# Performance work log

Hardware: AMD Instinct MI355X
Metric: run time of the kernel (lower is better)

The kernel has to match this reference:

```python
import jax, jax.numpy as jnp
import numpy as np

E, N, D, DFF, NE = 8, 4096, 1024, 2048, 65536

def setup_inputs() -> dict:
    key = jax.random.key(0)
    k1, k2, k3, k4 = jax.random.split(key, 4)
    x = jax.random.normal(k1, (E, N, D), dtype=jnp.float32)
    W1 = jax.random.normal(k2, (E, D, DFF), dtype=jnp.float32) * (1.0 / np.sqrt(D))
    W2 = jax.random.normal(k3, (E, DFF, D), dtype=jnp.float32) * (1.0 / np.sqrt(DFF))
    edge_index = jax.random.randint(k4, (2, NE), 0, N, dtype=jnp.int64)
    return {"x": x, "W1": W1, "W2": W2, "edge_index": edge_index}

def reference(x, W1, W2, edge_index):
    # Vectorized form of the per-expert Python loop + stack:
    # each expert: h = relu(x_e @ W1_e); agg[dst] += h[src]; out_e = agg @ W2_e
    n = x.shape[1]
    src, dst = edge_index[0], edge_index[1]
    h = jax.nn.relu(jnp.einsum('end,edf->enf', x, W1))  # [e, n, dff]
    msgs = h[:, src, :]                                  # [e, n_edges, dff] (irregular gather)
    agg = jax.vmap(lambda m: jax.ops.segment_sum(m, dst, num_segments=n))(msgs)  # [e, n, dff]
    out = jnp.einsum('enf,efd->end', agg, W2)            # [e, n, d] == x.shape
    return out
```

## Files before the change

kernel.cpp:

```cpp
#include <hip/hip_runtime.h>

#define E_ 8
#define N_ 4096
#define D_ 1024
#define DFF_ 2048
#define NE_ 65536

typedef __attribute__((ext_vector_type(8))) short short8;
typedef __attribute__((ext_vector_type(4))) float f32x4;

__device__ __forceinline__ unsigned short f2bf(float f) {
  unsigned u = __float_as_uint(f);
  u += 0x7fffu + ((u >> 16) & 1u);
  return (unsigned short)(u >> 16);
}
__device__ __forceinline__ float bf2f(unsigned short h) {
  return __uint_as_float(((unsigned)h) << 16);
}


__global__ __launch_bounds__(256) void cvt_f32_bf16_vec(
    const float* __restrict__ in, unsigned short* __restrict__ out, int n4) {
  int i = blockIdx.x * 256 + threadIdx.x;
  if (i >= n4) return;
  float4 v = ((const float4*)in)[i];
  ushort4 o;
  o.x = f2bf(v.x); o.y = f2bf(v.y); o.z = f2bf(v.z); o.w = f2bf(v.w);
  ((ushort4*)out)[i] = o;
}

__global__ __launch_bounds__(256) void transpose_cvt(
    const float* __restrict__ in, unsigned short* __restrict__ out, int R, int C) {
  __shared__ float tile[32][33];
  const int e = blockIdx.z;
  const float* ine = in + (size_t)e * R * C;
  unsigned short* oute = out + (size_t)e * R * C;
  const int c0 = blockIdx.x * 32, r0 = blockIdx.y * 32;
  const int tx = threadIdx.x & 31, ty = threadIdx.x >> 5;
#pragma unroll
  for (int i = 0; i < 32; i += 8)
    tile[ty + i][tx] = ine[(size_t)(r0 + ty + i) * C + (c0 + tx)];
  __syncthreads();
#pragma unroll
  for (int i = 0; i < 32; i += 8)
    oute[(size_t)(c0 + ty + i) * R + (r0 + tx)] = f2bf(tile[tx][ty + i]);
}


__global__ __launch_bounds__(256) void zero_i32(int* __restrict__ p, int n) {
  int i = blockIdx.x * 256 + threadIdx.x;
  if (i < n) p[i] = 0;
}

__global__ __launch_bounds__(256) void hist_dst(
    const int* __restrict__ ei, int* __restrict__ cnt, int ne) {
  int i = blockIdx.x * 256 + threadIdx.x;
  if (i < ne) atomicAdd(&cnt[ei[ne + i]], 1);
}

__global__ __launch_bounds__(1024) void scan4096(
    const int* __restrict__ cnt, int* __restrict__ rowptr, int* __restrict__ cursor) {
  __shared__ int tmp[1024];
  const int tid = threadIdx.x;
  const int b = tid * 4;
  int c0 = cnt[b + 0], c1 = cnt[b + 1], c2 = cnt[b + 2], c3 = cnt[b + 3];
  int tot = c0 + c1 + c2 + c3;
  tmp[tid] = tot;
  __syncthreads();
  int val = tot;
  for (int off = 1; off < 1024; off <<= 1) {
    int v = 0;
    if (tid >= off) v = tmp[tid - off];
    __syncthreads();
    val += v;
    tmp[tid] = val;
    __syncthreads();
  }
  const int excl = val - tot;
  rowptr[b + 0] = excl;
  rowptr[b + 1] = excl + c0;
  rowptr[b + 2] = excl + c0 + c1;
  rowptr[b + 3] = excl + c0 + c1 + c2;
  cursor[b + 0] = excl;
  cursor[b + 1] = excl + c0;
  cursor[b + 2] = excl + c0 + c1;
  cursor[b + 3] = excl + c0 + c1 + c2;
  if (tid == 1023) rowptr[N_] = val;
}

__global__ __launch_bounds__(256) void fill_csr(
    const int* __restrict__ ei, int* __restrict__ cursor, int* __restrict__ csr, int ne) {
  int i = blockIdx.x * 256 + threadIdx.x;
  if (i < ne) {
    int s = ei[i];
    int d = ei[ne + i];
    int pos = atomicAdd(&cursor[d], 1);
    csr[pos] = s;
  }
}


#define BAR() asm volatile("s_barrier" ::: "memory")
#define WAIT_LGKM0() asm volatile("s_waitcnt lgkmcnt(0)" ::: "memory")
#define WAIT_VM(n) asm volatile("s_waitcnt vmcnt(" #n ")" ::: "memory")

#define ALDS(buf, h) ((((buf) << 1) | (h)) * 16384)
#define BLDS(buf, h) (65536 + (((buf) << 1) | (h)) * 16384)

template <bool RELU>
__global__ __launch_bounds__(512, 1) void gemm256(
    const unsigned short* __restrict__ A, const unsigned short* __restrict__ BT,
    unsigned short* __restrict__ Cb, int M, int Nm, int K, int nbx, int nbxy) {
  __shared__ char lds[131072];

  const int orig = blockIdx.x;
  const int sw = (orig & 7) * nbxy + (orig >> 3);
  const int e = sw / nbxy;
  const int rem = sw - e * nbxy;
  const int by = rem / nbx;
  const int bx = rem - by * nbx;
  const int m0 = by * 256, n0 = bx * 256;

  const int tid = threadIdx.x;
  const int lane = tid & 63;
  const int wid = tid >> 6;
  const int wm = wid >> 2;
  const int wn = wid & 3;
  const int lo = lane & 15, hi = lane >> 4;

  const unsigned short* Ae = A + (size_t)e * M * K;
  const unsigned short* Be = BT + (size_t)e * Nm * K;
  unsigned short* Ce = Cb + (size_t)e * M * Nm;

  const unsigned short* Abase = Ae + (size_t)m0 * K;
  const unsigned short* Bbase = Be + (size_t)n0 * K;
  const size_t khalf = (size_t)128 * K;

  const int s1 = tid + 512;
  const int r0s = tid >> 3, c0s = (tid & 7) ^ (r0s & 7);
  const int r1s = s1 >> 3, c1s = (s1 & 7) ^ (r1s & 7);
  const int eo0 = r0s * K + c0s * 8;
  const int eo1 = r1s * K + c1s * 8;

#define STAGE(gbase_, ldsoff_)                                                             \
  do {                                                                                     \
    __builtin_amdgcn_global_load_lds(                                                      \
        (const __attribute__((address_space(1))) void*)((gbase_) + eo0),                   \
        (__attribute__((address_space(3))) void*)(lds + (ldsoff_) + wid * 1024), 16, 0, 0);\
    __builtin_amdgcn_global_load_lds(                                                      \
        (const __attribute__((address_space(1))) void*)((gbase_) + eo1),                   \
        (__attribute__((address_space(3))) void*)(lds + (ldsoff_) + 8192 + wid * 1024),    \
        16, 0, 0);                                                                         \
  } while (0)

  const int a_ks0 = lo * 128 + (((0 + hi) ^ (lo & 7)) << 4);
  const int a_ks1 = lo * 128 + (((4 + hi) ^ (lo & 7)) << 4);
  const int bfrag_base = (wn & 1) * 8192;

  f32x4 acc[8][4];
#pragma unroll
  for (int i = 0; i < 8; ++i)
#pragma unroll
    for (int j = 0; j < 4; ++j) acc[i][j] = (f32x4){0.f, 0.f, 0.f, 0.f};

  short8 af[8][2], bfr[2][2];

  auto loadA = [&](const char* Ah) {
#pragma unroll
    for (int fm = 0; fm < 8; ++fm) {
      af[fm][0] = *(const short8*)(Ah + a_ks0 + fm * 2048);
      af[fm][1] = *(const short8*)(Ah + a_ks1 + fm * 2048);
    }
  };
  auto loadB = [&](const char* Bh, int f0) {
#pragma unroll
    for (int j = 0; j < 2; ++j) {
      bfr[j][0] = *(const short8*)(Bh + a_ks0 + (f0 + j) * 2048);
      bfr[j][1] = *(const short8*)(Bh + a_ks1 + (f0 + j) * 2048);
    }
  };
  auto quad = [&](int FM0, int FN0) {
    __builtin_amdgcn_s_setprio(1);
#pragma unroll
    for (int fm = 0; fm < 4; ++fm)
#pragma unroll
      for (int j = 0; j < 2; ++j) {
        acc[FM0 + fm][FN0 + j] = __builtin_amdgcn_mfma_f32_16x16x32_bf16(
            af[FM0 + fm][0], bfr[j][0], acc[FM0 + fm][FN0 + j], 0, 0, 0);
        acc[FM0 + fm][FN0 + j] = __builtin_amdgcn_mfma_f32_16x16x32_bf16(
            af[FM0 + fm][1], bfr[j][1], acc[FM0 + fm][FN0 + j], 0, 0, 0);
      }
    __builtin_amdgcn_s_setprio(0);
  };

  const int nkt = K >> 6;

  STAGE(Abase, ALDS(0, 0));
  STAGE(Abase + khalf, ALDS(0, 1));
  STAGE(Bbase, BLDS(0, 0));
  STAGE(Bbase + khalf, BLDS(0, 1));
  STAGE(Abase + 64, ALDS(1, 0));
  STAGE(Abase + khalf + 64, ALDS(1, 1));
  STAGE(Bbase + 64, BLDS(1, 0));
  WAIT_VM(6);
  BAR();

  for (int t = 0; t < nkt; ++t) {
    const int buf = t & 1;
    const char* Ah = lds + ALDS(buf, wm);
    const char* Bh = lds + BLDS(buf, wn >> 1) + bfrag_base;

    loadA(Ah);
    loadB(Bh, 0);
    if (t + 1 < nkt) STAGE(Bbase + khalf + (size_t)(t + 1) * 64, BLDS((t + 1) & 1, 1));
    BAR();
    WAIT_LGKM0();
    quad(0, 0);
    BAR();

    if (t + 2 < nkt) STAGE(Abase + (size_t)(t + 2) * 64, ALDS(buf, 0));
    BAR();
    quad(4, 0);
    BAR();

    loadB(Bh, 2);
    if (t + 2 < nkt) STAGE(Abase + khalf + (size_t)(t + 2) * 64, ALDS(buf, 1));
    BAR();
    WAIT_LGKM0();
    quad(0, 2);
    BAR();

    if (t + 2 < nkt) STAGE(Bbase + (size_t)(t + 2) * 64, BLDS(buf, 0));
    BAR();
    quad(4, 2);
    if (t + 2 < nkt) {
      WAIT_VM(6);
    } else {
      WAIT_VM(0);
    }
    BAR();
  }

  const int row0 = m0 + wm * 128 + hi * 4;
  const int col0 = n0 + wn * 64 + lo;
#pragma unroll
  for (int fm = 0; fm < 8; ++fm)
#pragma unroll
    for (int fn = 0; fn < 4; ++fn)
#pragma unroll
      for (int r = 0; r < 4; ++r) {
        float v = acc[fm][fn][r];
        if (RELU) v = fmaxf(v, 0.f);
        Ce[(size_t)(row0 + fm * 16 + r) * Nm + (col0 + fn * 16)] = f2bf(v);
      }
#undef STAGE
}


__global__ __launch_bounds__(256) void gather_sum(
    const unsigned short* __restrict__ y, const int* __restrict__ rowptr,
    const int* __restrict__ csr, float* __restrict__ out) {
  const int dst = blockIdx.x;
  const int e = blockIdx.y;
  const unsigned short* ye = y + (size_t)e * N_ * D_;
  float* oute = out + (size_t)e * N_ * D_ + (size_t)dst * D_;
  const int t = threadIdx.x;
  const int beg = rowptr[dst], end = rowptr[dst + 1];
  float a0 = 0.f, a1 = 0.f, a2 = 0.f, a3 = 0.f;
  for (int i = beg; i < end; ++i) {
    const int s = csr[i];
    ushort4 v = ((const ushort4*)(ye + (size_t)s * D_))[t];
    a0 += bf2f(v.x);
    a1 += bf2f(v.y);
    a2 += bf2f(v.z);
    a3 += bf2f(v.w);
  }
  float4 o;
  o.x = a0; o.y = a1; o.z = a2; o.w = a3;
  ((float4*)oute)[t] = o;
}


extern "C" void kernel_launch(void* const* d_in, const int* in_sizes, int n_in,
                              void* d_out, int out_size, void* d_ws, size_t ws_size,
                              hipStream_t stream) {
  (void)in_sizes; (void)n_in; (void)out_size; (void)ws_size;
  const float* x = (const float*)d_in[0];
  const float* W1 = (const float*)d_in[1];
  const float* W2 = (const float*)d_in[2];
  const int* ei = (const int*)d_in[3];
  float* out = (float*)d_out;

  char* p = (char*)d_ws;
  auto alloc = [&](size_t b) {
    char* r = p;
    p += (b + 255) & ~(size_t)255;
    return r;
  };
  unsigned short* xbf = (unsigned short*)alloc((size_t)E_ * N_ * D_ * 2);
  unsigned short* w1t = (unsigned short*)alloc((size_t)E_ * D_ * DFF_ * 2);
  unsigned short* w2t = (unsigned short*)alloc((size_t)E_ * DFF_ * D_ * 2);
  unsigned short* h = (unsigned short*)alloc((size_t)E_ * N_ * DFF_ * 2);
  unsigned short* y = (unsigned short*)alloc((size_t)E_ * N_ * D_ * 2);
  int* cnt = (int*)alloc((size_t)N_ * 4);
  int* rowptr = (int*)alloc((size_t)(N_ + 1) * 4);
  int* cursor = (int*)alloc((size_t)N_ * 4);
  int* csr = (int*)alloc((size_t)NE_ * 4);

  cvt_f32_bf16_vec<<<(E_ * N_ * D_ / 4 + 255) / 256, 256, 0, stream>>>(x, xbf, E_ * N_ * D_ / 4);
  transpose_cvt<<<dim3(DFF_ / 32, D_ / 32, E_), 256, 0, stream>>>(W1, w1t, D_, DFF_);
  transpose_cvt<<<dim3(D_ / 32, DFF_ / 32, E_), 256, 0, stream>>>(W2, w2t, DFF_, D_);

  zero_i32<<<(N_ + 255) / 256, 256, 0, stream>>>(cnt, N_);
  hist_dst<<<NE_ / 256, 256, 0, stream>>>(ei, cnt, NE_);
  scan4096<<<1, 1024, 0, stream>>>(cnt, rowptr, cursor);
  fill_csr<<<NE_ / 256, 256, 0, stream>>>(ei, cursor, csr, NE_);

  {
    int nbx = DFF_ / 256, nby = N_ / 256;
    gemm256<true><<<nbx * nby * E_, 512, 0, stream>>>(xbf, w1t, h, N_, DFF_, D_, nbx, nbx * nby);
  }
  {
    int nbx = D_ / 256, nby = N_ / 256;
    gemm256<false><<<nbx * nby * E_, 512, 0, stream>>>(h, w2t, y, N_, D_, DFF_, nbx, nbx * nby);
  }

  gather_sum<<<dim3(N_, E_), 256, 0, stream>>>(y, rowptr, csr, out);
}
```

Before: 484.3 us.

## Restructure bf16 GEMM into 4-stage K=32 LDS ring with single barrier per tile

Changes the GEMM main loop from a double-buffered K=64 schedule with half-tile staging and several barriers per iteration to a 4-buffer ring of K=32 tiles. Each tile is prefetched three iterations ahead and needs only one barrier per step. The LDS layout and swizzle are redesigned so each wave reads its A/B fragments with one 16-byte load per fragment, and the setprio hints are dropped. This aims to cut barrier and synchronisation overhead and hide more load latency, at the cost of twice as many loop iterations and a new swizzle that may cause bank conflicts.

```diff
diff --git a/kernel.cpp b/kernel.cpp
--- a/kernel.cpp
+++ b/kernel.cpp
@@ -101,11 +101,7 @@
 
 
 #define BAR() asm volatile("s_barrier" ::: "memory")
-#define WAIT_LGKM0() asm volatile("s_waitcnt lgkmcnt(0)" ::: "memory")
 #define WAIT_VM(n) asm volatile("s_waitcnt vmcnt(" #n ")" ::: "memory")
-
-#define ALDS(buf, h) ((((buf) << 1) | (h)) * 16384)
-#define BLDS(buf, h) (65536 + (((buf) << 1) | (h)) * 16384)
 
 template <bool RELU>
 __global__ __launch_bounds__(512, 1) void gemm256(
@@ -128,34 +124,38 @@
   const int wn = wid & 3;
   const int lo = lane & 15, hi = lane >> 4;
 
-  const unsigned short* Ae = A + (size_t)e * M * K;
-  const unsigned short* Be = BT + (size_t)e * Nm * K;
+  const unsigned short* Ae = A + (size_t)e * M * K + (size_t)m0 * K;
+  const unsigned short* Be = BT + (size_t)e * Nm * K + (size_t)n0 * K;
   unsigned short* Ce = Cb + (size_t)e * M * Nm;
 
-  const unsigned short* Abase = Ae + (size_t)m0 * K;
-  const unsigned short* Bbase = Be + (size_t)n0 * K;
-  const size_t khalf = (size_t)128 * K;
-
-  const int s1 = tid + 512;
-  const int r0s = tid >> 3, c0s = (tid & 7) ^ (r0s & 7);
-  const int r1s = s1 >> 3, c1s = (s1 & 7) ^ (r1s & 7);
-  const int eo0 = r0s * K + c0s * 8;
-  const int eo1 = r1s * K + c1s * 8;
-
-#define STAGE(gbase_, ldsoff_)                                                             \
-  do {                                                                                     \
-    __builtin_amdgcn_global_load_lds(                                                      \
-        (const __attribute__((address_space(1))) void*)((gbase_) + eo0),                   \
-        (__attribute__((address_space(3))) void*)(lds + (ldsoff_) + wid * 1024), 16, 0, 0);\
-    __builtin_amdgcn_global_load_lds(                                                      \
-        (const __attribute__((address_space(1))) void*)((gbase_) + eo1),                   \
-        (__attribute__((address_space(3))) void*)(lds + (ldsoff_) + 8192 + wid * 1024),    \
-        16, 0, 0);                                                                         \
+  auto srcoff = [&](int p) -> size_t {
+    int R = p >> 3, s = p & 7;
+    int bc = s ^ (R & 7);
+    int gr = 2 * R + (bc >> 2), c = bc & 3;
+    return (size_t)gr * K + (size_t)c * 8;
+  };
+  const size_t so0 = srcoff(tid);
+  const size_t so1 = srcoff(tid + 512);
+
+#define GLD(src_, dst_)                                                        \
+  __builtin_amdgcn_global_load_lds(                                            \
+      (const __attribute__((address_space(1))) void*)(src_),                   \
+      (__attribute__((address_space(3))) void*)(dst_), 16, 0, 0)
+
+#define STAGE(t_)                                                              \
+  do {                                                                         \
+    char* Lb_ = lds + ((t_) & 3) * 32768;                                      \
+    const unsigned short* ga_ = Ae + (size_t)(t_) * 32;                        \
+    const unsigned short* gb_ = Be + (size_t)(t_) * 32;                        \
+    GLD(ga_ + so0, Lb_ + tid * 16);                                            \
+    GLD(ga_ + so1, Lb_ + 8192 + tid * 16);                                     \
+    GLD(gb_ + so0, Lb_ + 16384 + tid * 16);                                    \
+    GLD(gb_ + so1, Lb_ + 24576 + tid * 16);                                    \
   } while (0)
 
-  const int a_ks0 = lo * 128 + (((0 + hi) ^ (lo & 7)) << 4);
-  const int a_ks1 = lo * 128 + (((4 + hi) ^ (lo & 7)) << 4);
-  const int bfrag_base = (wn & 1) * 8192;
+  const int slot = (((lo & 1) << 2) | hi) ^ ((lo >> 1) & 7);
+  const int aoff = (wm * 64 + (lo >> 1)) * 128 + slot * 16;
+  const int boff = 16384 + (wn * 32 + (lo >> 1)) * 128 + slot * 16;
 
   f32x4 acc[8][4];
 #pragma unroll
@@ -163,83 +163,37 @@
 #pragma unroll
     for (int j = 0; j < 4; ++j) acc[i][j] = (f32x4){0.f, 0.f, 0.f, 0.f};
 
-  short8 af[8][2], bfr[2][2];
-
-  auto loadA = [&](const char* Ah) {
-#pragma unroll
-    for (int fm = 0; fm < 8; ++fm) {
-      af[fm][0] = *(const short8*)(Ah + a_ks0 + fm * 2048);
-      af[fm][1] = *(const short8*)(Ah + a_ks1 + fm * 2048);
-    }
+  auto tile_body = [&](int t, bool dostage) {
+    const char* L = lds + (t & 3) * 32768;
+    short8 af[8], bfv[4];
+#pragma unroll
+    for (int fm = 0; fm < 8; ++fm) af[fm] = *(const short8*)(L + aoff + fm * 1024);
+#pragma unroll
+    for (int fn = 0; fn < 4; ++fn) bfv[fn] = *(const short8*)(L + boff + fn * 1024);
+    if (dostage) STAGE(t + 3);
+#pragma unroll
+    for (int fm = 0; fm < 8; ++fm)
+#pragma unroll
+      for (int fn = 0; fn < 4; ++fn)
+        acc[fm][fn] = __builtin_amdgcn_mfma_f32_16x16x32_bf16(af[fm], bfv[fn],
+                                                              acc[fm][fn], 0, 0, 0);
   };
-  auto loadB = [&](const char* Bh, int f0) {
-#pragma unroll
-    for (int j = 0; j < 2; ++j) {
-      bfr[j][0] = *(const short8*)(Bh + a_ks0 + (f0 + j) * 2048);
-      bfr[j][1] = *(const short8*)(Bh + a_ks1 + (f0 + j) * 2048);
-    }
-  };
-  auto quad = [&](int FM0, int FN0) {
-    __builtin_amdgcn_s_setprio(1);
-#pragma unroll
-    for (int fm = 0; fm < 4; ++fm)
-#pragma unroll
-      for (int j = 0; j < 2; ++j) {
-        acc[FM0 + fm][FN0 + j] = __builtin_amdgcn_mfma_f32_16x16x32_bf16(
-            af[FM0 + fm][0], bfr[j][0], acc[FM0 + fm][FN0 + j], 0, 0, 0);
-        acc[FM0 + fm][FN0 + j] = __builtin_amdgcn_mfma_f32_16x16x32_bf16(
-            af[FM0 + fm][1], bfr[j][1], acc[FM0 + fm][FN0 + j], 0, 0, 0);
-      }
-    __builtin_amdgcn_s_setprio(0);
-  };
-
-  const int nkt = K >> 6;
-
-  STAGE(Abase, ALDS(0, 0));
-  STAGE(Abase + khalf, ALDS(0, 1));
-  STAGE(Bbase, BLDS(0, 0));
-  STAGE(Bbase + khalf, BLDS(0, 1));
-  STAGE(Abase + 64, ALDS(1, 0));
-  STAGE(Abase + khalf + 64, ALDS(1, 1));
-  STAGE(Bbase + 64, BLDS(1, 0));
-  WAIT_VM(6);
-  BAR();
-
-  for (int t = 0; t < nkt; ++t) {
-    const int buf = t & 1;
-    const char* Ah = lds + ALDS(buf, wm);
-    const char* Bh = lds + BLDS(buf, wn >> 1) + bfrag_base;
-
-    loadA(Ah);
-    loadB(Bh, 0);
-    if (t + 1 < nkt) STAGE(Bbase + khalf + (size_t)(t + 1) * 64, BLDS((t + 1) & 1, 1));
+
+  const int nkt = K >> 5;
+
+  STAGE(0);
+  STAGE(1);
+  STAGE(2);
+
+  int t = 0;
+  for (; t < nkt - 3; ++t) {
+    WAIT_VM(8);
     BAR();
-    WAIT_LGKM0();
-    quad(0, 0);
-    BAR();
-
-    if (t + 2 < nkt) STAGE(Abase + (size_t)(t + 2) * 64, ALDS(buf, 0));
-    BAR();
-    quad(4, 0);
-    BAR();
-
-    loadB(Bh, 2);
-    if (t + 2 < nkt) STAGE(Abase + khalf + (size_t)(t + 2) * 64, ALDS(buf, 1));
-    BAR();
-    WAIT_LGKM0();
-    quad(0, 2);
-    BAR();
-
-    if (t + 2 < nkt) STAGE(Bbase + (size_t)(t + 2) * 64, BLDS(buf, 0));
-    BAR();
-    quad(4, 2);
-    if (t + 2 < nkt) {
-      WAIT_VM(6);
-    } else {
-      WAIT_VM(0);
-    }
-    BAR();
-  }
+    tile_body(t, true);
+  }
+  WAIT_VM(8); BAR(); tile_body(nkt - 3, false);
+  WAIT_VM(4); BAR(); tile_body(nkt - 2, false);
+  WAIT_VM(0); BAR(); tile_body(nkt - 1, false);
 
   const int row0 = m0 + wm * 128 + hi * 4;
   const int col0 = n0 + wn * 64 + lo;
@@ -254,6 +208,7 @@
         Ce[(size_t)(row0 + fm * 16 + r) * Nm + (col0 + fn * 16)] = f2bf(v);
       }
 #undef STAGE
+#undef GLD
 }
 
 
```

After: 500.5 us. 1.03x slower.
